# Kernel tuning notes

Measured on AMD Instinct MI355X. Metric: run time of the kernel, lower is better.

## Reference

```python
import jax, jax.numpy as jnp
import numpy as np

EMBED_DIM = 1024
NUM_HEADS = 16
D_K = EMBED_DIM // NUM_HEADS


def setup_inputs() -> dict:
    key = jax.random.key(0)
    ks = jax.random.split(key, 5)
    s = 1.0 / np.sqrt(EMBED_DIM)  # roughly match nn.Linear init scale
    return {
        "x": jax.random.normal(ks[0], (2, 2048, EMBED_DIM), dtype=jnp.float32),
        "wq": jax.random.normal(ks[1], (EMBED_DIM, EMBED_DIM), dtype=jnp.float32) * s,
        "wk": jax.random.normal(ks[2], (EMBED_DIM, EMBED_DIM), dtype=jnp.float32) * s,
        "wv": jax.random.normal(ks[3], (EMBED_DIM, EMBED_DIM), dtype=jnp.float32) * s,
        "wo": jax.random.normal(ks[4], (EMBED_DIM, EMBED_DIM), dtype=jnp.float32) * s,
    }


def reference(x, wq, wk, wv, wo):
    b, s, e = x.shape
    # nn.Linear(bias=False): y = x @ W.T
    def split_heads(t):
        return t.reshape(b, s, NUM_HEADS, D_K).transpose(0, 2, 1, 3)  # [b,h,s,d]
    q = split_heads(x @ wq.T)
    k = split_heads(x @ wk.T)
    v = split_heads(x @ wv.T)
    scores = jnp.einsum("bhqd,bhkd->bhqk", q, k) / jnp.sqrt(jnp.float32(D_K))
    attn = jax.nn.softmax(scores, axis=-1)
    out = jnp.einsum("bhqk,bhkd->bhqd", attn, v)  # [b,h,s,d]
    out = out.transpose(0, 2, 1, 3).reshape(b, s, e)
    return out @ wo.T
```

## Files before the change

kernel.cpp:

```cpp
#include <hip/hip_runtime.h>
#include <stdint.h>

typedef unsigned short u16;
typedef float f32x4 __attribute__((ext_vector_type(4)));
typedef __bf16 bf16x8 __attribute__((ext_vector_type(8)));
typedef short s16x4 __attribute__((ext_vector_type(4)));

__device__ __forceinline__ u16 f2bf(float f) {
  union { float f; uint32_t u; } c; c.f = f;
  uint32_t u = c.u;
  u += 0x7fffu + ((u >> 16) & 1u);
  return (u16)(u >> 16);
}

__device__ __forceinline__ uint32_t pkbf(float a, float b) {
  union { float f; uint32_t u; } ua, ub; ua.f = a; ub.f = b;
  return __builtin_amdgcn_perm(ub.u, ua.u, 0x07060302u);
}

#define GLOAD_LDS16(g, l)                                                              \
  __builtin_amdgcn_global_load_lds((__attribute__((address_space(1))) void*)(g),       \
                                   (__attribute__((address_space(3))) void*)(l), 16, 0, 0)

__global__ __launch_bounds__(256) void cvt_all(const float* __restrict__ x,
                                               const float* __restrict__ wq,
                                               const float* __restrict__ wk,
                                               const float* __restrict__ wv,
                                               const float* __restrict__ wo,
                                               u16* __restrict__ xb,
                                               u16* __restrict__ wqkvb,
                                               u16* __restrict__ wob) {
  int bx = blockIdx.x;
  const float* src;
  u16* dst;
  int i;
  if (bx < 4096) {
    src = x; dst = xb; i = bx * 256 + threadIdx.x;
  } else {
    int r = bx - 4096;
    int w = r >> 10;
    i = (r & 1023) * 256 + threadIdx.x;
    if (w == 0)      { src = wq; dst = wqkvb; }
    else if (w == 1) { src = wk; dst = wqkvb + 1048576; }
    else if (w == 2) { src = wv; dst = wqkvb + 2097152; }
    else             { src = wo; dst = wob; }
  }
  const float4 v = ((const float4*)src)[i];
  ushort4 o;
  o.x = f2bf(v.x); o.y = f2bf(v.y); o.z = f2bf(v.z); o.w = f2bf(v.w);
  ((ushort4*)dst)[i] = o;
}

__global__ __launch_bounds__(256) void gemm_qkv(const u16* __restrict__ A,
                                                const u16* __restrict__ B,
                                                u16* __restrict__ QKb,
                                                u16* __restrict__ Vt) {
  const int K = 1024;
  __shared__ __align__(16) u16 sA[128 * 32];
  __shared__ __align__(16) u16 sB[128 * 32];
  const int tid = threadIdx.x;
  const int lane = tid & 63;
  const int wave = tid >> 6;
  const int quad = lane >> 4, l16 = lane & 15;
  const int wm = (wave >> 1) * 64, wn = (wave & 1) * 64;
  const int bm = blockIdx.y * 128, bn = blockIdx.x * 128;

  const int ar = tid >> 2;
  const int ac = (tid & 3) * 8;

  f32x4 acc[4][4];
#pragma unroll
  for (int i = 0; i < 4; i++)
#pragma unroll
    for (int j = 0; j < 4; j++) acc[i][j] = (f32x4){0.f, 0.f, 0.f, 0.f};

  const u16* pA0 = A + (size_t)(bm + ar) * K + ac;
  const u16* pA1 = A + (size_t)(bm + 64 + ar) * K + ac;
  const u16* pB0 = B + (size_t)(bn + ar) * K + ac;
  const u16* pB1 = B + (size_t)(bn + 64 + ar) * K + ac;

  for (int k0 = 0; k0 < K; k0 += 32) {
    GLOAD_LDS16(pA0 + k0, (char*)sA + tid * 16);
    GLOAD_LDS16(pA1 + k0, (char*)sA + 4096 + tid * 16);
    GLOAD_LDS16(pB0 + k0, (char*)sB + tid * 16);
    GLOAD_LDS16(pB1 + k0, (char*)sB + 4096 + tid * 16);
    __syncthreads();
    bf16x8 af[4], bfr[4];
#pragma unroll
    for (int mt = 0; mt < 4; mt++)
      af[mt] = *(const bf16x8*)&sA[(wm + mt * 16 + l16) * 32 + quad * 8];
#pragma unroll
    for (int nt = 0; nt < 4; nt++)
      bfr[nt] = *(const bf16x8*)&sB[(wn + nt * 16 + l16) * 32 + quad * 8];
#pragma unroll
    for (int mt = 0; mt < 4; mt++)
#pragma unroll
      for (int nt = 0; nt < 4; nt++)
        acc[mt][nt] = __builtin_amdgcn_mfma_f32_16x16x32_bf16(af[mt], bfr[nt], acc[mt][nt], 0, 0, 0);
    __syncthreads();
  }

  if (blockIdx.x < 16) {
    const float qs = (blockIdx.x < 8) ? 0.18033688011f : 1.0f;
#pragma unroll
    for (int mt = 0; mt < 4; mt++)
#pragma unroll
      for (int nt = 0; nt < 4; nt++)
#pragma unroll
        for (int r = 0; r < 4; r++) {
          int row = bm + wm + mt * 16 + quad * 4 + r;
          int col = bn + wn + nt * 16 + l16;
          QKb[(size_t)row * 2048 + col] = f2bf(acc[mt][nt][r] * qs);
        }
  } else {
#pragma unroll
    for (int mt = 0; mt < 4; mt++)
#pragma unroll
      for (int nt = 0; nt < 4; nt++) {
        int hd = (bn - 2048) + wn + nt * 16 + l16;
        int tok = bm + wm + mt * 16 + quad * 4;
        ushort4 o;
        o.x = f2bf(acc[mt][nt][0]);
        o.y = f2bf(acc[mt][nt][1]);
        o.z = f2bf(acc[mt][nt][2]);
        o.w = f2bf(acc[mt][nt][3]);
        *(ushort4*)&Vt[(size_t)hd * 4096 + tok] = o;
      }
  }
}

__global__ __launch_bounds__(256, 3) void attn_fwd(const u16* __restrict__ QKb,
                                                   const u16* __restrict__ Vt,
                                                   u16* __restrict__ O) {
  const int bx = blockIdx.x;
  const int qt = bx >> 5;
  const int h  = (bx >> 1) & 15;
  const int b  = bx & 1;
  const int tid = threadIdx.x;
  const int lane = tid & 63;
  const int wave = tid >> 6;
  const int quad = lane >> 4, l16 = lane & 15;

  __shared__ __align__(16) u16 smem[24576];
  u16* sK0 = smem;
  u16* sK1 = smem + 4096;
  u16* sV0 = smem + 8192;
  u16* sV1 = smem + 12288;
  u16* sQ  = smem + 16384;

  const int tok0 = b * 2048;
  const int q0 = qt * 128;
  const int colh = h * 64;

#pragma unroll
  for (int k2 = 0; k2 < 4; k2++) {
    int c = k2 * 256 + tid;
    int row = c >> 3, c8 = (c & 7) ^ (row & 7);
    GLOAD_LDS16(QKb + (size_t)(tok0 + q0 + row) * 2048 + colh + c8 * 8,
                (char*)sQ + c * 16);
  }
#pragma unroll
  for (int k2 = 0; k2 < 2; k2++) {
    int c = k2 * 256 + tid;
    int row = c >> 3, c8 = (c & 7) ^ (row & 7);
    GLOAD_LDS16(QKb + (size_t)(tok0 + row) * 2048 + 1024 + colh + c8 * 8,
                (char*)sK0 + c * 16);
    GLOAD_LDS16(Vt + (size_t)(colh + row) * 4096 + tok0 + c8 * 8,
                (char*)sV0 + c * 16);
  }
  __syncthreads();

  bf16x8 aq[2][2];
#pragma unroll
  for (int sub = 0; sub < 2; sub++)
#pragma unroll
    for (int kh = 0; kh < 2; kh++) {
      int row = wave * 32 + sub * 16 + l16;
      aq[sub][kh] = *(const bf16x8*)&sQ[row * 64 + (((kh * 4 + quad) ^ (row & 7)) * 8)];
    }

  f32x4 oacc[2][4];
  float lsum[2] = {0.f, 0.f};
#pragma unroll
  for (int sub = 0; sub < 2; sub++)
#pragma unroll
    for (int db = 0; db < 4; db++) oacc[sub][db] = (f32x4){0.f, 0.f, 0.f, 0.f};

  int p = 0;
  for (int it = 0; it < 32; ++it) {
    u16* sKc = p ? sK1 : sK0;
    u16* sVc = p ? sV1 : sV0;
    if (it < 31) {
      u16* sKn = p ? sK0 : sK1;
      u16* sVn = p ? sV0 : sV1;
      const int nkv = (it + 1) * 64;
#pragma unroll
      for (int k2 = 0; k2 < 2; k2++) {
        int c = k2 * 256 + tid;
        int row = c >> 3, c8 = (c & 7) ^ (row & 7);
        GLOAD_LDS16(QKb + (size_t)(tok0 + nkv + row) * 2048 + 1024 + colh + c8 * 8,
                    (char*)sKn + c * 16);
        GLOAD_LDS16(Vt + (size_t)(colh + row) * 4096 + tok0 + nkv + c8 * 8,
                    (char*)sVn + c * 16);
      }
    }

    bf16x8 kf[4][2];
#pragma unroll
    for (int nt = 0; nt < 4; nt++)
#pragma unroll
      for (int kh = 0; kh < 2; kh++) {
        int rr = nt * 16 + l16;
        kf[nt][kh] = *(const bf16x8*)&sKc[rr * 64 + (((kh * 4 + quad) ^ (rr & 7)) * 8)];
      }
    s16x4 vf[4][4];
#pragma unroll
    for (int db = 0; db < 4; db++)
#pragma unroll
      for (int nt = 0; nt < 4; nt++) {
        int row = db * 16 + l16;
        int c16 = (nt * 2 + (quad >> 1)) ^ (row & 7);
        vf[db][nt] = *(const s16x4*)&sVc[row * 64 + c16 * 8 + (quad & 1) * 4];
      }

#pragma unroll
    for (int sub = 0; sub < 2; sub++) {
      float e[4][4];
#pragma unroll
      for (int nt = 0; nt < 4; nt++) {
        f32x4 c = (f32x4){0.f, 0.f, 0.f, 0.f};
        c = __builtin_amdgcn_mfma_f32_16x16x32_bf16(kf[nt][0], aq[sub][0], c, 0, 0, 0);
        c = __builtin_amdgcn_mfma_f32_16x16x32_bf16(kf[nt][1], aq[sub][1], c, 0, 0, 0);
#pragma unroll
        for (int r = 0; r < 4; r++) e[nt][r] = __builtin_amdgcn_exp2f(c[r]);
        lsum[sub] += (e[nt][0] + e[nt][1]) + (e[nt][2] + e[nt][3]);
      }
#pragma unroll
      for (int nt = 0; nt < 4; nt++) {
        union { uint32_t u[2]; s16x4 v; } bb;
        bb.u[0] = pkbf(e[nt][0], e[nt][1]);
        bb.u[1] = pkbf(e[nt][2], e[nt][3]);
#pragma unroll
        for (int db = 0; db < 4; db++)
          oacc[sub][db] = __builtin_amdgcn_mfma_f32_16x16x16bf16_1k(vf[db][nt], bb.v, oacc[sub][db], 0, 0, 0);
      }
    }
    __syncthreads();
    p ^= 1;
  }

#pragma unroll
  for (int sub = 0; sub < 2; sub++) {
    float v = lsum[sub];
    v += __shfl_xor(v, 16, 64);
    v += __shfl_xor(v, 32, 64);
    lsum[sub] = 1.0f / v;
  }

  u16* sT = smem + wave * 6144;
#pragma unroll
  for (int sub = 0; sub < 2; sub++)
#pragma unroll
    for (int db = 0; db < 4; db++)
#pragma unroll
      for (int r = 0; r < 4; r++)
        sT[(sub * 16 + l16) * 68 + db * 16 + quad * 4 + r] = f2bf(oacc[sub][db][r] * lsum[sub]);
#pragma unroll
  for (int k = 0; k < 4; k++) {
    int qrow = k * 8 + (lane >> 3);
    int cch = lane & 7;
    uint4 vrow = *(const uint4*)&sT[qrow * 68 + cch * 8];
    int tokr = tok0 + q0 + wave * 32 + qrow;
    *(uint4*)&O[(size_t)tokr * 1024 + colh + cch * 8] = vrow;
  }
}

__global__ __launch_bounds__(256) void gemm_out(const u16* __restrict__ A,
                                                const u16* __restrict__ B,
                                                float* __restrict__ C) {
  const int N = 1024, K = 1024;
  __shared__ __align__(16) u16 sA[128 * 32];
  __shared__ __align__(16) u16 sB[64 * 32];
  const int tid = threadIdx.x;
  const int lane = tid & 63;
  const int wave = tid >> 6;
  const int quad = lane >> 4, l16 = lane & 15;
  const int wm = (wave >> 1) * 64, wn = (wave & 1) * 32;
  const int bm = blockIdx.y * 128, bn = blockIdx.x * 64;
  const int ar = tid >> 2;
  const int ac = (tid & 3) * 8;

  f32x4 acc[4][2];
#pragma unroll
  for (int i = 0; i < 4; i++)
#pragma unroll
    for (int j = 0; j < 2; j++) acc[i][j] = (f32x4){0.f, 0.f, 0.f, 0.f};

  const u16* pA0 = A + (size_t)(bm + ar) * K + ac;
  const u16* pA1 = A + (size_t)(bm + 64 + ar) * K + ac;
  const u16* pB0 = B + (size_t)(bn + ar) * K + ac;

  for (int k0 = 0; k0 < K; k0 += 32) {
    GLOAD_LDS16(pA0 + k0, (char*)sA + tid * 16);
    GLOAD_LDS16(pA1 + k0, (char*)sA + 4096 + tid * 16);
    GLOAD_LDS16(pB0 + k0, (char*)sB + tid * 16);
    __syncthreads();
    bf16x8 af[4], bfr[2];
#pragma unroll
    for (int mt = 0; mt < 4; mt++)
      af[mt] = *(const bf16x8*)&sA[(wm + mt * 16 + l16) * 32 + quad * 8];
#pragma unroll
    for (int nt = 0; nt < 2; nt++)
      bfr[nt] = *(const bf16x8*)&sB[(wn + nt * 16 + l16) * 32 + quad * 8];
#pragma unroll
    for (int mt = 0; mt < 4; mt++)
#pragma unroll
      for (int nt = 0; nt < 2; nt++)
        acc[mt][nt] = __builtin_amdgcn_mfma_f32_16x16x32_bf16(af[mt], bfr[nt], acc[mt][nt], 0, 0, 0);
    __syncthreads();
  }

#pragma unroll
  for (int mt = 0; mt < 4; mt++)
#pragma unroll
    for (int nt = 0; nt < 2; nt++)
#pragma unroll
      for (int r = 0; r < 4; r++) {
        int row = bm + wm + mt * 16 + quad * 4 + r;
        int col = bn + wn + nt * 16 + l16;
        C[(size_t)row * N + col] = acc[mt][nt][r];
      }
}

extern "C" void kernel_launch(void* const* d_in, const int* in_sizes, int n_in,
                              void* d_out, int out_size, void* d_ws, size_t ws_size,
                              hipStream_t stream) {
  const float* x  = (const float*)d_in[0];
  const float* wq = (const float*)d_in[1];
  const float* wk = (const float*)d_in[2];
  const float* wv = (const float*)d_in[3];
  const float* wo = (const float*)d_in[4];
  float* out = (float*)d_out;
  char* ws = (char*)d_ws;
  const size_t MB = 1u << 20;

  u16* xb    = (u16*)(ws);
  u16* wqkvb = (u16*)(ws + 8 * MB);
  u16* wob   = (u16*)(ws + 14 * MB);
  u16* QKb   = (u16*)(ws + 16 * MB);
  u16* Vtb   = (u16*)(ws + 32 * MB);
  u16* Ob    = xb;

  cvt_all<<<8192, 256, 0, stream>>>(x, wq, wk, wv, wo, xb, wqkvb, wob);

  gemm_qkv<<<dim3(24, 32), 256, 0, stream>>>(xb, wqkvb, QKb, Vtb);

  attn_fwd<<<512, 256, 0, stream>>>(QKb, Vtb, Ob);

  gemm_out<<<dim3(16, 32), 256, 0, stream>>>(Ob, wob, out);
}
```

Baseline: 194.8 us.

## Deepen GEMM K-tile to 64 with swizzled LDS; halve attention query tile

Both projection GEMMs now load a 64-wide K slice per iteration into XOR-swizzled LDS. This halves the number of barrier pairs and cuts LDS bank conflicts on fragment reads, at the cost of doubling shared memory per block. The attention kernel drops from 128 to 64 query rows per block, with one 16-row sub-tile per wave, and launches 1024 blocks with a min-blocks-per-CU hint of 4. That gives more blocks to fill the CUs and lighter register and LDS use per block, but each block now reloads K/V for half as many queries, so K/V global traffic doubles.

Measured after the change: 192.1 us. About the same (-1.3%).

```diff
diff --git a/kernel.cpp b/kernel.cpp
--- a/kernel.cpp
+++ b/kernel.cpp
@@ -56,8 +56,8 @@
                                                 u16* __restrict__ QKb,
                                                 u16* __restrict__ Vt) {
   const int K = 1024;
-  __shared__ __align__(16) u16 sA[128 * 32];
-  __shared__ __align__(16) u16 sB[128 * 32];
+  __shared__ __align__(16) u16 sA[128 * 64];
+  __shared__ __align__(16) u16 sB[128 * 64];
   const int tid = threadIdx.x;
   const int lane = tid & 63;
   const int wave = tid >> 6;
@@ -65,38 +65,38 @@
   const int wm = (wave >> 1) * 64, wn = (wave & 1) * 64;
   const int bm = blockIdx.y * 128, bn = blockIdx.x * 128;
 
-  const int ar = tid >> 2;
-  const int ac = (tid & 3) * 8;
-
   f32x4 acc[4][4];
 #pragma unroll
   for (int i = 0; i < 4; i++)
 #pragma unroll
     for (int j = 0; j < 4; j++) acc[i][j] = (f32x4){0.f, 0.f, 0.f, 0.f};
 
-  const u16* pA0 = A + (size_t)(bm + ar) * K + ac;
-  const u16* pA1 = A + (size_t)(bm + 64 + ar) * K + ac;
-  const u16* pB0 = B + (size_t)(bn + ar) * K + ac;
-  const u16* pB1 = B + (size_t)(bn + 64 + ar) * K + ac;
-
-  for (int k0 = 0; k0 < K; k0 += 32) {
-    GLOAD_LDS16(pA0 + k0, (char*)sA + tid * 16);
-    GLOAD_LDS16(pA1 + k0, (char*)sA + 4096 + tid * 16);
-    GLOAD_LDS16(pB0 + k0, (char*)sB + tid * 16);
-    GLOAD_LDS16(pB1 + k0, (char*)sB + 4096 + tid * 16);
-    __syncthreads();
-    bf16x8 af[4], bfr[4];
-#pragma unroll
-    for (int mt = 0; mt < 4; mt++)
-      af[mt] = *(const bf16x8*)&sA[(wm + mt * 16 + l16) * 32 + quad * 8];
-#pragma unroll
-    for (int nt = 0; nt < 4; nt++)
-      bfr[nt] = *(const bf16x8*)&sB[(wn + nt * 16 + l16) * 32 + quad * 8];
-#pragma unroll
-    for (int mt = 0; mt < 4; mt++)
-#pragma unroll
-      for (int nt = 0; nt < 4; nt++)
-        acc[mt][nt] = __builtin_amdgcn_mfma_f32_16x16x32_bf16(af[mt], bfr[nt], acc[mt][nt], 0, 0, 0);
+  for (int k0 = 0; k0 < K; k0 += 64) {
+#pragma unroll
+    for (int k2 = 0; k2 < 4; k2++) {
+      int c = k2 * 256 + tid;
+      int row = c >> 3, c8 = (c & 7) ^ (row & 7);
+      GLOAD_LDS16(A + (size_t)(bm + row) * K + k0 + c8 * 8, (char*)sA + c * 16);
+      GLOAD_LDS16(B + (size_t)(bn + row) * K + k0 + c8 * 8, (char*)sB + c * 16);
+    }
+    __syncthreads();
+    bf16x8 af[4][2], bfr[4][2];
+#pragma unroll
+    for (int mt = 0; mt < 4; mt++)
+#pragma unroll
+      for (int kh = 0; kh < 2; kh++) {
+        int ra = wm + mt * 16 + l16;
+        af[mt][kh] = *(const bf16x8*)&sA[ra * 64 + (((kh * 4 + quad) ^ (ra & 7)) * 8)];
+        int rb = wn + mt * 16 + l16;
+        bfr[mt][kh] = *(const bf16x8*)&sB[rb * 64 + (((kh * 4 + quad) ^ (rb & 7)) * 8)];
+      }
+#pragma unroll
+    for (int mt = 0; mt < 4; mt++)
+#pragma unroll
+      for (int nt = 0; nt < 4; nt++) {
+        acc[mt][nt] = __builtin_amdgcn_mfma_f32_16x16x32_bf16(af[mt][0], bfr[nt][0], acc[mt][nt], 0, 0, 0);
+        acc[mt][nt] = __builtin_amdgcn_mfma_f32_16x16x32_bf16(af[mt][1], bfr[nt][1], acc[mt][nt], 0, 0, 0);
+      }
     __syncthreads();
   }
 
@@ -129,7 +129,7 @@
   }
 }
 
-__global__ __launch_bounds__(256, 3) void attn_fwd(const u16* __restrict__ QKb,
+__global__ __launch_bounds__(256, 4) void attn_fwd(const u16* __restrict__ QKb,
                                                    const u16* __restrict__ Vt,
                                                    u16* __restrict__ O) {
   const int bx = blockIdx.x;
@@ -141,7 +141,7 @@
   const int wave = tid >> 6;
   const int quad = lane >> 4, l16 = lane & 15;
 
-  __shared__ __align__(16) u16 smem[24576];
+  __shared__ __align__(16) u16 smem[20480];
   u16* sK0 = smem;
   u16* sK1 = smem + 4096;
   u16* sV0 = smem + 8192;
@@ -149,11 +149,11 @@
   u16* sQ  = smem + 16384;
 
   const int tok0 = b * 2048;
-  const int q0 = qt * 128;
+  const int q0 = qt * 64;
   const int colh = h * 64;
 
 #pragma unroll
-  for (int k2 = 0; k2 < 4; k2++) {
+  for (int k2 = 0; k2 < 2; k2++) {
     int c = k2 * 256 + tid;
     int row = c >> 3, c8 = (c & 7) ^ (row & 7);
     GLOAD_LDS16(QKb + (size_t)(tok0 + q0 + row) * 2048 + colh + c8 * 8,
@@ -170,21 +170,17 @@
   }
   __syncthreads();
 
-  bf16x8 aq[2][2];
-#pragma unroll
-  for (int sub = 0; sub < 2; sub++)
-#pragma unroll
-    for (int kh = 0; kh < 2; kh++) {
-      int row = wave * 32 + sub * 16 + l16;
-      aq[sub][kh] = *(const bf16x8*)&sQ[row * 64 + (((kh * 4 + quad) ^ (row & 7)) * 8)];
-    }
-
-  f32x4 oacc[2][4];
-  float lsum[2] = {0.f, 0.f};
-#pragma unroll
-  for (int sub = 0; sub < 2; sub++)
-#pragma unroll
-    for (int db = 0; db < 4; db++) oacc[sub][db] = (f32x4){0.f, 0.f, 0.f, 0.f};
+  bf16x8 aq[2];
+#pragma unroll
+  for (int kh = 0; kh < 2; kh++) {
+    int row = wave * 16 + l16;
+    aq[kh] = *(const bf16x8*)&sQ[row * 64 + (((kh * 4 + quad) ^ (row & 7)) * 8)];
+  }
+
+  f32x4 oacc[4];
+  float lsum = 0.f;
+#pragma unroll
+  for (int db = 0; db < 4; db++) oacc[db] = (f32x4){0.f, 0.f, 0.f, 0.f};
 
   int p = 0;
   for (int it = 0; it < 32; ++it) {
@@ -223,54 +219,48 @@
         vf[db][nt] = *(const s16x4*)&sVc[row * 64 + c16 * 8 + (quad & 1) * 4];
       }
 
-#pragma unroll
-    for (int sub = 0; sub < 2; sub++) {
-      float e[4][4];
-#pragma unroll
-      for (int nt = 0; nt < 4; nt++) {
-        f32x4 c = (f32x4){0.f, 0.f, 0.f, 0.f};
-        c = __builtin_amdgcn_mfma_f32_16x16x32_bf16(kf[nt][0], aq[sub][0], c, 0, 0, 0);
-        c = __builtin_amdgcn_mfma_f32_16x16x32_bf16(kf[nt][1], aq[sub][1], c, 0, 0, 0);
-#pragma unroll
-        for (int r = 0; r < 4; r++) e[nt][r] = __builtin_amdgcn_exp2f(c[r]);
-        lsum[sub] += (e[nt][0] + e[nt][1]) + (e[nt][2] + e[nt][3]);
-      }
-#pragma unroll
-      for (int nt = 0; nt < 4; nt++) {
-        union { uint32_t u[2]; s16x4 v; } bb;
-        bb.u[0] = pkbf(e[nt][0], e[nt][1]);
-        bb.u[1] = pkbf(e[nt][2], e[nt][3]);
-#pragma unroll
-        for (int db = 0; db < 4; db++)
-          oacc[sub][db] = __builtin_amdgcn_mfma_f32_16x16x16bf16_1k(vf[db][nt], bb.v, oacc[sub][db], 0, 0, 0);
-      }
+    float e[4][4];
+#pragma unroll
+    for (int nt = 0; nt < 4; nt++) {
+      f32x4 c = (f32x4){0.f, 0.f, 0.f, 0.f};
+      c = __builtin_amdgcn_mfma_f32_16x16x32_bf16(kf[nt][0], aq[0], c, 0, 0, 0);
+      c = __builtin_amdgcn_mfma_f32_16x16x32_bf16(kf[nt][1], aq[1], c, 0, 0, 0);
+#pragma unroll
+      for (int r = 0; r < 4; r++) e[nt][r] = __builtin_amdgcn_exp2f(c[r]);
+      lsum += (e[nt][0] + e[nt][1]) + (e[nt][2] + e[nt][3]);
+    }
+#pragma unroll
+    for (int nt = 0; nt < 4; nt++) {
+      union { uint32_t u[2]; s16x4 v; } bb;
+      bb.u[0] = pkbf(e[nt][0], e[nt][1]);
+      bb.u[1] = pkbf(e[nt][2], e[nt][3]);
+#pragma unroll
+      for (int db = 0; db < 4; db++)
+        oacc[db] = __builtin_amdgcn_mfma_f32_16x16x16bf16_1k(vf[db][nt], bb.v, oacc[db], 0, 0, 0);
     }
     __syncthreads();
     p ^= 1;
   }
 
-#pragma unroll
-  for (int sub = 0; sub < 2; sub++) {
-    float v = lsum[sub];
+  {
+    float v = lsum;
     v += __shfl_xor(v, 16, 64);
     v += __shfl_xor(v, 32, 64);
-    lsum[sub] = 1.0f / v;
-  }
-
-  u16* sT = smem + wave * 6144;
-#pragma unroll
-  for (int sub = 0; sub < 2; sub++)
-#pragma unroll
-    for (int db = 0; db < 4; db++)
-#pragma unroll
-      for (int r = 0; r < 4; r++)
-        sT[(sub * 16 + l16) * 68 + db * 16 + quad * 4 + r] = f2bf(oacc[sub][db][r] * lsum[sub]);
-#pragma unroll
-  for (int k = 0; k < 4; k++) {
+    lsum = 1.0f / v;
+  }
+
+  u16* sT = smem + wave * 1088;
+#pragma unroll
+  for (int db = 0; db < 4; db++)
+#pragma unroll
+    for (int r = 0; r < 4; r++)
+      sT[l16 * 68 + db * 16 + quad * 4 + r] = f2bf(oacc[db][r] * lsum);
+#pragma unroll
+  for (int k = 0; k < 2; k++) {
     int qrow = k * 8 + (lane >> 3);
     int cch = lane & 7;
     uint4 vrow = *(const uint4*)&sT[qrow * 68 + cch * 8];
-    int tokr = tok0 + q0 + wave * 32 + qrow;
+    int tokr = tok0 + q0 + wave * 16 + qrow;
     *(uint4*)&O[(size_t)tokr * 1024 + colh + cch * 8] = vrow;
   }
 }
@@ -279,16 +269,14 @@
                                                 const u16* __restrict__ B,
                                                 float* __restrict__ C) {
   const int N = 1024, K = 1024;
-  __shared__ __align__(16) u16 sA[128 * 32];
-  __shared__ __align__(16) u16 sB[64 * 32];
+  __shared__ __align__(16) u16 sA[128 * 64];
+  __shared__ __align__(16) u16 sB[64 * 64];
   const int tid = threadIdx.x;
   const int lane = tid & 63;
   const int wave = tid >> 6;
   const int quad = lane >> 4, l16 = lane & 15;
   const int wm = (wave >> 1) * 64, wn = (wave & 1) * 32;
   const int bm = blockIdx.y * 128, bn = blockIdx.x * 64;
-  const int ar = tid >> 2;
-  const int ac = (tid & 3) * 8;
 
   f32x4 acc[4][2];
 #pragma unroll
@@ -296,27 +284,42 @@
 #pragma unroll
     for (int j = 0; j < 2; j++) acc[i][j] = (f32x4){0.f, 0.f, 0.f, 0.f};
 
-  const u16* pA0 = A + (size_t)(bm + ar) * K + ac;
-  const u16* pA1 = A + (size_t)(bm + 64 + ar) * K + ac;
-  const u16* pB0 = B + (size_t)(bn + ar) * K + ac;
-
-  for (int k0 = 0; k0 < K; k0 += 32) {
-    GLOAD_LDS16(pA0 + k0, (char*)sA + tid * 16);
-    GLOAD_LDS16(pA1 + k0, (char*)sA + 4096 + tid * 16);
-    GLOAD_LDS16(pB0 + k0, (char*)sB + tid * 16);
-    __syncthreads();
-    bf16x8 af[4], bfr[2];
-#pragma unroll
-    for (int mt = 0; mt < 4; mt++)
-      af[mt] = *(const bf16x8*)&sA[(wm + mt * 16 + l16) * 32 + quad * 8];
+  for (int k0 = 0; k0 < K; k0 += 64) {
+#pragma unroll
+    for (int k2 = 0; k2 < 4; k2++) {
+      int c = k2 * 256 + tid;
+      int row = c >> 3, c8 = (c & 7) ^ (row & 7);
+      GLOAD_LDS16(A + (size_t)(bm + row) * K + k0 + c8 * 8, (char*)sA + c * 16);
+    }
+#pragma unroll
+    for (int k2 = 0; k2 < 2; k2++) {
+      int c = k2 * 256 + tid;
+      int row = c >> 3, c8 = (c & 7) ^ (row & 7);
+      GLOAD_LDS16(B + (size_t)(bn + row) * K + k0 + c8 * 8, (char*)sB + c * 16);
+    }
+    __syncthreads();
+    bf16x8 af[4][2], bfr[2][2];
+#pragma unroll
+    for (int mt = 0; mt < 4; mt++)
+#pragma unroll
+      for (int kh = 0; kh < 2; kh++) {
+        int ra = wm + mt * 16 + l16;
+        af[mt][kh] = *(const bf16x8*)&sA[ra * 64 + (((kh * 4 + quad) ^ (ra & 7)) * 8)];
+      }
 #pragma unroll
     for (int nt = 0; nt < 2; nt++)
-      bfr[nt] = *(const bf16x8*)&sB[(wn + nt * 16 + l16) * 32 + quad * 8];
-#pragma unroll
-    for (int mt = 0; mt < 4; mt++)
-#pragma unroll
-      for (int nt = 0; nt < 2; nt++)
-        acc[mt][nt] = __builtin_amdgcn_mfma_f32_16x16x32_bf16(af[mt], bfr[nt], acc[mt][nt], 0, 0, 0);
+#pragma unroll
+      for (int kh = 0; kh < 2; kh++) {
+        int rb = wn + nt * 16 + l16;
+        bfr[nt][kh] = *(const bf16x8*)&sB[rb * 64 + (((kh * 4 + quad) ^ (rb & 7)) * 8)];
+      }
+#pragma unroll
+    for (int mt = 0; mt < 4; mt++)
+#pragma unroll
+      for (int nt = 0; nt < 2; nt++) {
+        acc[mt][nt] = __builtin_amdgcn_mfma_f32_16x16x32_bf16(af[mt][0], bfr[nt][0], acc[mt][nt], 0, 0, 0);
+        acc[mt][nt] = __builtin_amdgcn_mfma_f32_16x16x32_bf16(af[mt][1], bfr[nt][1], acc[mt][nt], 0, 0, 0);
+      }
     __syncthreads();
   }
 
@@ -355,7 +358,7 @@
 
   gemm_qkv<<<dim3(24, 32), 256, 0, stream>>>(xb, wqkvb, QKb, Vtb);
 
-  attn_fwd<<<512, 256, 0, stream>>>(QKb, Vtb, Ob);
+  attn_fwd<<<1024, 256, 0, stream>>>(QKb, Vtb, Ob);
 
   gemm_out<<<dim3(16, 32), 256, 0, stream>>>(Ob, wob, out);
 }
```
